# Performance work log

Measured on AMD Instinct MI355X. Metric: run time of the kernel, lower is better.

The kernel has to match this reference:

```python
import jax, jax.numpy as jnp
import numpy as np

N_EMBD = 1024
N_HEAD = 16
BASE_SCALE = 0.03125  # config.base_scale
ATTN_ALPHA_INIT = 0.05
MLP_ALPHA_INIT = 0.05
SQK_INIT = 1.0
SUV_INIT = 1.0


def justnorm(x):
    return x / jnp.linalg.norm(x, axis=-1, keepdims=True)


def normalized_linear(x, W):
    # F.normalize(weight, p=2, dim=0): unit-norm columns of W [out, in] across the out dim
    Wn = W / jnp.linalg.norm(W, axis=0, keepdims=True)
    return x @ Wn.T


def setup_inputs() -> dict:
    key = jax.random.key(0)
    ks = jax.random.split(key, 8)
    C = N_EMBD
    s = 1.0 / np.sqrt(C)
    inp = {
        "h": jax.random.normal(ks[0], (8, 1024, C), dtype=jnp.float32),
        "Wq": jax.random.normal(ks[1], (C, C), dtype=jnp.float32) * s,
        "Wk": jax.random.normal(ks[2], (C, C), dtype=jnp.float32) * s,
        "Wv": jax.random.normal(ks[3], (C, C), dtype=jnp.float32) * s,
        "Wo": jax.random.normal(ks[4], (C, C), dtype=jnp.float32) * s,
        "Wfc": jax.random.normal(ks[5], (8 * C, C), dtype=jnp.float32) * s,
        "Wproj": jax.random.normal(ks[6], (C, 4 * C), dtype=jnp.float32) * (1.0 / np.sqrt(4 * C)),
        "sqk": jnp.full((C,), SQK_INIT * BASE_SCALE, dtype=jnp.float32),
        "suv": jnp.full((8 * C,), SUV_INIT * 1.0, dtype=jnp.float32),
        "attn_alpha": jnp.full((C,), BASE_SCALE, dtype=jnp.float32),
        "mlp_alpha": jnp.full((C,), BASE_SCALE, dtype=jnp.float32),
    }
    return inp


def reference(h, Wq, Wk, Wv, Wo, Wfc, Wproj, sqk, suv, attn_alpha, mlp_alpha):
    B, T, C = h.shape
    H, D = N_HEAD, C // N_HEAD

    # ---- attention ----
    q = normalized_linear(h, Wq).reshape(B, T, H, D).transpose(0, 2, 1, 3)  # bhtd
    k = normalized_linear(h, Wk).reshape(B, T, H, D).transpose(0, 2, 1, 3)
    v = normalized_linear(h, Wv).reshape(B, T, H, D).transpose(0, 2, 1, 3)

    sqk_s = (sqk * (SQK_INIT / BASE_SCALE)).reshape(1, H, 1, D)  # per-(head, head_dim) scale
    q = sqk_s * justnorm(q)
    k = sqk_s * justnorm(k)

    softmax_scale = float(D) ** 0.5  # nGPT uses sqrt(head_dim)
    att = jax.nn.softmax(jnp.einsum("bhqd,bhkd->bhqk", q, k) * softmax_scale, axis=-1)
    y = jnp.einsum("bhqk,bhkd->bhqd", att, v)
    y = y.transpose(0, 2, 1, 3).reshape(B, T, C)
    h_att = normalized_linear(y, Wo)

    lr = jnp.abs(attn_alpha * (ATTN_ALPHA_INIT / BASE_SCALE))
    A = justnorm(h)
    Bn = justnorm(h_att)
    h = justnorm(A + lr * (Bn - A))

    # ---- SwiGLU MLP ----
    uv = h @ Wfc.T  # [B,T,8C]
    suv_s = suv * (SUV_INIT / 1.0 * (C ** 0.5))
    uv = suv_s * uv
    u, vg = jnp.split(uv, 2, axis=-1)
    x_mlp = u * jax.nn.silu(vg)
    h_mlp = x_mlp @ Wproj.T

    lr = jnp.abs(mlp_alpha * (MLP_ALPHA_INIT / BASE_SCALE))
    A = justnorm(h)
    Bn = justnorm(h_mlp)
    h = justnorm(A + lr * (Bn - A))
    return h
```

## Files before the change

### kernel.cpp

```cpp
#include <hip/hip_runtime.h>

typedef __attribute__((ext_vector_type(8))) short s8v;
typedef __attribute__((ext_vector_type(4))) short s4v;
typedef __attribute__((ext_vector_type(4))) float f4v;

__device__ __forceinline__ float b2f(unsigned short b) {
  union { unsigned u; float f; } x; x.u = ((unsigned)b) << 16; return x.f;
}
__device__ __forceinline__ unsigned short f2b(float f) {
  union { float f; unsigned u; } x; x.f = f;
  unsigned r = x.u + 0x7fffu + ((x.u >> 16) & 1u);
  return (unsigned short)(r >> 16);
}
__device__ __forceinline__ void gl_lds16(const void* g, void* l) {
  __builtin_amdgcn_global_load_lds(
      (const __attribute__((address_space(1))) unsigned int*)g,
      (__attribute__((address_space(3))) unsigned int*)l, 16, 0, 0);
}

__global__ void colsq(const float* __restrict__ W, float* __restrict__ out, int K) {
  int j = blockIdx.x * 256 + threadIdx.x;
  const float* p = W + (long)(blockIdx.y * 64) * K + j;
  float s = 0.f;
#pragma unroll 4
  for (int n = 0; n < 64; ++n) { float v = p[(long)n * K]; s += v * v; }
  atomicAdd(&out[j], s);
}

__global__ void convw(const float* __restrict__ src, const float* __restrict__ cs,
                      unsigned short* __restrict__ dst, int Kmask) {
  long idx = ((long)blockIdx.x * 256 + threadIdx.x) << 2;
  float4 v = *(const float4*)(src + idx);
  int j = (int)(idx & (long)Kmask);
  s4v o;
  o[0] = (short)f2b(v.x * rsqrtf(cs[j]));
  o[1] = (short)f2b(v.y * rsqrtf(cs[j + 1]));
  o[2] = (short)f2b(v.z * rsqrtf(cs[j + 2]));
  o[3] = (short)f2b(v.w * rsqrtf(cs[j + 3]));
  *(s4v*)(dst + idx) = o;
}

__global__ void castf2b(const float* __restrict__ src, unsigned short* __restrict__ dst) {
  long idx = ((long)blockIdx.x * 256 + threadIdx.x) << 2;
  float4 v = *(const float4*)(src + idx);
  s4v o;
  o[0] = (short)f2b(v.x); o[1] = (short)f2b(v.y);
  o[2] = (short)f2b(v.z); o[3] = (short)f2b(v.w);
  *(s4v*)(dst + idx) = o;
}

__global__ __launch_bounds__(256) void gemm_bt(
    const unsigned short* __restrict__ A, const unsigned short* __restrict__ B,
    unsigned short* __restrict__ Cout, int K, int ldc) {
  __shared__ unsigned short smem[32768];
  const int tid = threadIdx.x, lane = tid & 63, w = tid >> 6;
  const int quad = lane >> 4, lq = lane & 15;
  const int wy = w >> 1, wx = w & 1;
  const int m0 = blockIdx.y << 7, n0 = blockIdx.x << 7;

  const int trow = tid >> 2;
  const int cb = ((tid & 3) ^ ((tid >> 3) & 3)) << 3;
  const unsigned short* Ag0 = A + (long)(m0 + trow) * K + cb;
  const unsigned short* Ag1 = A + (long)(m0 + 64 + trow) * K + cb;
  const unsigned short* Bg0 = B + (long)(n0 + trow) * K + cb;
  const unsigned short* Bg1 = B + (long)(n0 + 64 + trow) * K + cb;
  unsigned short* l0 = smem + (tid << 3);

  const int swz = ((lq >> 1) & 3) << 4;
  const int aoff = (wy * 64 + lq) * 64 + ((quad << 4) ^ swz);
  const int boff = 8192 + (wx * 64 + lq) * 64 + ((quad << 4) ^ swz);

  f4v acc[4][4];
  f4v zero = {0.f, 0.f, 0.f, 0.f};
#pragma unroll
  for (int i = 0; i < 4; ++i)
#pragma unroll
    for (int j = 0; j < 4; ++j) acc[i][j] = zero;

  auto stage = [&](int T) {
    const int bo = (T & 3) << 13;
    const int col = T << 5;
    gl_lds16(Ag0 + col, l0 + bo);
    gl_lds16(Ag1 + col, l0 + bo + 2048);
    gl_lds16(Bg0 + col, l0 + bo + 4096);
    gl_lds16(Bg1 + col, l0 + bo + 6144);
  };
  const char* sb = (const char*)smem;
  auto compute = [&](int kt) {
    const int bo = (kt & 3) << 14;
    s8v a[4], b[4];
#pragma unroll
    for (int i = 0; i < 4; ++i) a[i] = *(const s8v*)(sb + bo + aoff + i * 1024);
#pragma unroll
    for (int j = 0; j < 4; ++j) b[j] = *(const s8v*)(sb + bo + boff + j * 1024);
    __builtin_amdgcn_s_setprio(1);
#pragma unroll
    for (int i = 0; i < 4; ++i)
#pragma unroll
      for (int j = 0; j < 4; ++j)
        acc[i][j] = __builtin_amdgcn_mfma_f32_16x16x32_bf16(a[i], b[j], acc[i][j], 0, 0, 0);
    __builtin_amdgcn_s_setprio(0);
  };

  const int nt = K >> 5;
  stage(0); stage(1); stage(2);
  for (int kt = 0; kt < nt - 2; ++kt) {
    asm volatile("s_waitcnt vmcnt(8)" ::: "memory");
    __builtin_amdgcn_s_barrier();
    asm volatile("" ::: "memory");
    if (kt < nt - 3) stage(kt + 3);
    compute(kt);
  }
  asm volatile("s_waitcnt vmcnt(4)" ::: "memory");
  __builtin_amdgcn_s_barrier();
  asm volatile("" ::: "memory");
  compute(nt - 2);
  asm volatile("s_waitcnt vmcnt(0)" ::: "memory");
  __builtin_amdgcn_s_barrier();
  asm volatile("" ::: "memory");
  compute(nt - 1);

  __syncthreads();
#pragma unroll
  for (int i = 0; i < 4; ++i)
#pragma unroll
    for (int j = 0; j < 4; ++j)
#pragma unroll
      for (int r = 0; r < 4; ++r) {
        int row = wy * 64 + i * 16 + quad * 4 + r;
        int col = wx * 64 + j * 16 + lq;
        smem[row * 136 + col] = f2b(acc[i][j][r]);
      }
  __syncthreads();
#pragma unroll
  for (int it = 0; it < 8; ++it) {
    int row = it * 16 + (tid >> 4);
    int col = (tid & 15) << 3;
    s8v v = *(const s8v*)(smem + row * 136 + col);
    *(s8v*)(Cout + (long)(m0 + row) * ldc + n0 + col) = v;
  }
}

__global__ __launch_bounds__(512, 2) void gemm_fc(
    const unsigned short* __restrict__ A, const unsigned short* __restrict__ B,
    unsigned short* __restrict__ X, const float* __restrict__ suv) {
  __shared__ unsigned short smem[65536];
  const int tid = threadIdx.x, lane = tid & 63, w = tid >> 6;
  const int quad = lane >> 4, lq = lane & 15;
  const int wy = w >> 2, wx = w & 3;
  const int bid = blockIdx.x;
  const int xr = bid & 7, xq = bid >> 3;
  const int m0 = ((xr << 2) | (xq & 3)) << 8;
  const int n0 = (xq >> 2) << 7;

  const int swz = ((lq >> 1) & 3) << 4;
  const int aoff = wy * 8192 + lq * 64 + ((quad * 16) ^ swz);
  const int boff = 16384 + wx * 2048 + lq * 64 + ((quad * 16) ^ swz);

  const int trow = tid >> 2;
  const int cb = ((tid & 3) ^ ((tid >> 3) & 3)) << 3;
  const unsigned short* Ag0 = A + (long)(m0 + trow) * 1024 + cb;
  const unsigned short* Ag1 = A + (long)(m0 + 128 + trow) * 1024 + cb;
  const unsigned short* Bg0 = B + (long)(n0 + trow) * 1024 + cb;
  const unsigned short* Bg1 = B + (long)(4096 + n0 + trow) * 1024 + cb;
  unsigned short* l0 = smem + (tid << 3);

  float su[2], sv[2];
#pragma unroll
  for (int j = 0; j < 2; ++j) {
    su[j] = suv[n0 + wx * 32 + j * 16 + lq] * 32.f;
    sv[j] = suv[4096 + n0 + wx * 32 + j * 16 + lq] * 32.f;
  }

  f4v aU[8][2], aV[8][2];
  f4v zero = {0.f, 0.f, 0.f, 0.f};
#pragma unroll
  for (int m = 0; m < 8; ++m)
#pragma unroll
    for (int j = 0; j < 2; ++j) { aU[m][j] = zero; aV[m][j] = zero; }

  auto stage = [&](int T) {
    const int bo = (T & 3) << 14;
    const int col = T << 5;
    gl_lds16(Ag0 + col, l0 + bo);
    gl_lds16(Ag1 + col, l0 + bo + 4096);
    gl_lds16(Bg0 + col, l0 + bo + 8192);
    gl_lds16(Bg1 + col, l0 + bo + 12288);
  };

  const char* sb = (const char*)smem;
  auto compute = [&](int kt) {
    const int bo = (kt & 3) << 15;
    s8v bu0 = *(const s8v*)(sb + bo + boff);
    s8v bu1 = *(const s8v*)(sb + bo + boff + 1024);
    s8v bv0 = *(const s8v*)(sb + bo + boff + 8192);
    s8v bv1 = *(const s8v*)(sb + bo + boff + 9216);
    s8v av[8];
#pragma unroll
    for (int m = 0; m < 8; ++m) av[m] = *(const s8v*)(sb + bo + aoff + m * 1024);
    __builtin_amdgcn_s_setprio(1);
#pragma unroll
    for (int m = 0; m < 8; ++m) {
      aU[m][0] = __builtin_amdgcn_mfma_f32_16x16x32_bf16(av[m], bu0, aU[m][0], 0, 0, 0);
      aV[m][0] = __builtin_amdgcn_mfma_f32_16x16x32_bf16(av[m], bv0, aV[m][0], 0, 0, 0);
      aU[m][1] = __builtin_amdgcn_mfma_f32_16x16x32_bf16(av[m], bu1, aU[m][1], 0, 0, 0);
      aV[m][1] = __builtin_amdgcn_mfma_f32_16x16x32_bf16(av[m], bv1, aV[m][1], 0, 0, 0);
    }
    __builtin_amdgcn_s_setprio(0);
  };

  stage(0); stage(1); stage(2);
  for (int kt = 0; kt < 30; ++kt) {
    asm volatile("s_waitcnt vmcnt(8)" ::: "memory");
    __builtin_amdgcn_s_barrier();
    asm volatile("" ::: "memory");
    if (kt < 29) stage(kt + 3);
    compute(kt);
  }
  asm volatile("s_waitcnt vmcnt(4)" ::: "memory");
  __builtin_amdgcn_s_barrier();
  asm volatile("" ::: "memory");
  compute(30);
  asm volatile("s_waitcnt vmcnt(0)" ::: "memory");
  __builtin_amdgcn_s_barrier();
  asm volatile("" ::: "memory");
  compute(31);

  __syncthreads();
#pragma unroll
  for (int m = 0; m < 8; ++m)
#pragma unroll
    for (int j = 0; j < 2; ++j)
#pragma unroll
      for (int r = 0; r < 4; ++r) {
        int row = wy * 128 + m * 16 + quad * 4 + r;
        int col = wx * 32 + j * 16 + lq;
        float uu = aU[m][j][r] * su[j];
        float vg = aV[m][j][r] * sv[j];
        float sig = 1.f / (1.f + __builtin_amdgcn_exp2f(vg * -1.44269504f));
        smem[row * 132 + col] = f2b(uu * vg * sig);
      }
  __syncthreads();
  {
    const int row = tid >> 1, half = tid & 1;
    unsigned short* dst = X + (long)(m0 + row) * 4096 + n0 + half * 64;
    const unsigned short* srcr = smem + row * 132 + half * 64;
#pragma unroll
    for (int s = 0; s < 8; ++s)
      *(s8v*)(dst + s * 8) = *(const s8v*)(srcr + s * 8);
  }
}

__global__ __launch_bounds__(256) void qkv_norm(unsigned short* __restrict__ qkv,
                                                unsigned short* __restrict__ Vt,
                                                const float* __restrict__ sqk) {
  __shared__ unsigned short tl[64][72];
  const int tid = threadIdx.x;
  const int blk = blockIdx.x;
  const int tt = blk & 15, bh = blk >> 4, b = bh >> 4, h = bh & 15;
  const int t0 = tt << 6;
  const int r = tid >> 2, seg = tid & 3;
  float sc[16];
#pragma unroll
  for (int c = 0; c < 16; ++c) sc[c] = sqk[h * 64 + seg * 16 + c] * 32.f;
  for (int which = 0; which < 2; ++which) {
    unsigned short* p = qkv + (long)(b * 1024 + t0 + r) * 3072 + which * 1024 + h * 64 + seg * 16;
    s8v x0 = *(const s8v*)p, x1 = *(const s8v*)(p + 8);
    float ss = 0.f;
#pragma unroll
    for (int c = 0; c < 8; ++c) {
      float a = b2f((unsigned short)x0[c]), bb = b2f((unsigned short)x1[c]);
      ss += a * a + bb * bb;
    }
    ss += __shfl_xor(ss, 1, 64);
    ss += __shfl_xor(ss, 2, 64);
    float rn = rsqrtf(ss);
#pragma unroll
    for (int c = 0; c < 8; ++c) {
      x0[c] = (short)f2b(b2f((unsigned short)x0[c]) * rn * sc[c]);
      x1[c] = (short)f2b(b2f((unsigned short)x1[c]) * rn * sc[c + 8]);
    }
    *(s8v*)p = x0; *(s8v*)(p + 8) = x1;
  }
  {
    const unsigned short* p = qkv + (long)(b * 1024 + t0 + r) * 3072 + 2048 + h * 64 + seg * 16;
    s8v v0 = *(const s8v*)p, v1 = *(const s8v*)(p + 8);
#pragma unroll
    for (int c = 0; c < 8; ++c) {
      tl[seg * 16 + c][r] = (unsigned short)v0[c];
      tl[seg * 16 + 8 + c][r] = (unsigned short)v1[c];
    }
  }
  __syncthreads();
  {
    const int d = tid >> 2, part = tid & 3;
    s8v o0 = *(const s8v*)(&tl[d][part * 16]);
    s8v o1 = *(const s8v*)(&tl[d][part * 16 + 8]);
    unsigned short* q = Vt + (long)(bh * 64 + d) * 1024 + t0 + part * 16;
    *(s8v*)q = o0; *(s8v*)(q + 8) = o1;
  }
}

__global__ __launch_bounds__(256) void attn(const unsigned short* __restrict__ qkv,
                                            const unsigned short* __restrict__ Vt,
                                            unsigned short* __restrict__ Y) {
  __shared__ unsigned short smem[33792];
  unsigned short* Klds = smem;
  unsigned short* Vlds = smem + 8192;
  unsigned short* Plds = smem + 16384;
  const int tid = threadIdx.x, lane = tid & 63, w = tid >> 6;
  const int quad = lane >> 4, lq = lane & 15;
  const int bh = blockIdx.x, b = bh >> 4, h = bh & 15;
  const int qt = blockIdx.y;
  const int e0 = tid << 3;
  const int c_lo = e0 >> 10, row_s = (e0 & 1023) >> 3;
  const int vc_lo = e0 >> 9, vd = (e0 & 511) >> 3;

  s8v qf[2][2];
#pragma unroll
  for (int i = 0; i < 2; ++i)
#pragma unroll
    for (int ks = 0; ks < 2; ++ks) {
      int row = qt * 128 + w * 32 + i * 16 + lq;
      qf[i][ks] = *(const s8v*)(qkv + (long)(b * 1024 + row) * 3072 + h * 64 + ks * 32 + quad * 8);
    }

  f4v o[2][4];
  float lp[2][4];
  f4v zero = {0.f, 0.f, 0.f, 0.f};
#pragma unroll
  for (int i = 0; i < 2; ++i) {
#pragma unroll
    for (int nf = 0; nf < 4; ++nf) o[i][nf] = zero;
#pragma unroll
    for (int r = 0; r < 4; ++r) lp[i][r] = 0.f;
  }

  const unsigned short* Kg = qkv + (long)(b * 1024 + row_s) * 3072 + 1024 + h * 64 + (c_lo << 3);
  const unsigned short* Vg = Vt + (long)(bh * 64 + vd) * 1024 + (vc_lo << 3);
  unsigned short* Pw = Plds + w * 4352;

  for (int kt0 = 0; kt0 < 1024; kt0 += 128) {
    __syncthreads();
#pragma unroll
    for (int it = 0; it < 4; ++it) {
      gl_lds16(Kg + (long)kt0 * 3072 + it * 16, Klds + it * 2048 + e0);
      gl_lds16(Vg + kt0 + it * 32, Vlds + it * 2048 + e0);
    }
    __syncthreads();
    f4v s[2][8];
#pragma unroll
    for (int i = 0; i < 2; ++i)
#pragma unroll
      for (int j = 0; j < 8; ++j) s[i][j] = zero;
#pragma unroll
    for (int ks = 0; ks < 2; ++ks)
#pragma unroll
      for (int j = 0; j < 8; ++j) {
        s8v kf = *(const s8v*)(Klds + (ks * 4 + quad) * 1024 + (j * 16 + lq) * 8);
        s[0][j] = __builtin_amdgcn_mfma_f32_16x16x32_bf16(qf[0][ks], kf, s[0][j], 0, 0, 0);
        s[1][j] = __builtin_amdgcn_mfma_f32_16x16x32_bf16(qf[1][ks], kf, s[1][j], 0, 0, 0);
      }
#pragma unroll
    for (int i = 0; i < 2; ++i)
#pragma unroll
      for (int j = 0; j < 8; ++j)
#pragma unroll
        for (int r = 0; r < 4; ++r) {
          float p = __builtin_amdgcn_exp2f(s[i][j][r] * 11.5415603f - 11.5415603f);
          lp[i][r] += p;
          Pw[(i * 16 + quad * 4 + r) * 136 + j * 16 + lq] = f2b(p);
        }
    s8v pf[2][4];
#pragma unroll
    for (int i = 0; i < 2; ++i)
#pragma unroll
      for (int ks = 0; ks < 4; ++ks)
        pf[i][ks] = *(const s8v*)(Pw + (i * 16 + lq) * 136 + ks * 32 + quad * 8);
#pragma unroll
    for (int nf = 0; nf < 4; ++nf)
#pragma unroll
      for (int ks = 0; ks < 4; ++ks) {
        s8v vf = *(const s8v*)(Vlds + (ks * 4 + quad) * 512 + (nf * 16 + lq) * 8);
        o[0][nf] = __builtin_amdgcn_mfma_f32_16x16x32_bf16(pf[0][ks], vf, o[0][nf], 0, 0, 0);
        o[1][nf] = __builtin_amdgcn_mfma_f32_16x16x32_bf16(pf[1][ks], vf, o[1][nf], 0, 0, 0);
      }
  }
#pragma unroll
  for (int i = 0; i < 2; ++i)
#pragma unroll
    for (int r = 0; r < 4; ++r) {
      float v = lp[i][r];
      v += __shfl_xor(v, 1, 64); v += __shfl_xor(v, 2, 64);
      v += __shfl_xor(v, 4, 64); v += __shfl_xor(v, 8, 64);
      lp[i][r] = 1.f / v;
    }
#pragma unroll
  for (int i = 0; i < 2; ++i)
#pragma unroll
    for (int nf = 0; nf < 4; ++nf)
#pragma unroll
      for (int r = 0; r < 4; ++r) {
        int row = qt * 128 + w * 32 + i * 16 + quad * 4 + r;
        Y[(long)(b * 1024 + row) * 1024 + h * 64 + nf * 16 + lq] = f2b(o[i][nf][r] * lp[i][r]);
      }
}

__global__ __launch_bounds__(256) void residual(
    const float* __restrict__ hin, const unsigned short* __restrict__ hbr,
    const float* __restrict__ alpha, float* __restrict__ outf,
    unsigned short* __restrict__ outb) {
  __shared__ float red[8];
  const int tid = threadIdx.x, lane = tid & 63, w = tid >> 6;
  const long base = (long)blockIdx.x * 1024;
  float hv[4], bvv[4];
  float s1 = 0.f, s2 = 0.f;
#pragma unroll
  for (int k = 0; k < 4; ++k) {
    int c = k * 256 + tid;
    hv[k] = hin[base + c];
    bvv[k] = b2f(hbr[base + c]);
    s1 += hv[k] * hv[k]; s2 += bvv[k] * bvv[k];
  }
#pragma unroll
  for (int m = 1; m < 64; m <<= 1) { s1 += __shfl_xor(s1, m, 64); s2 += __shfl_xor(s2, m, 64); }
  if (lane == 0) { red[w] = s1; red[4 + w] = s2; }
  __syncthreads();
  s1 = red[0] + red[1] + red[2] + red[3];
  s2 = red[4] + red[5] + red[6] + red[7];
  float rn1 = rsqrtf(s1), rn2 = rsqrtf(s2);
  float z[4], s3 = 0.f;
#pragma unroll
  for (int k = 0; k < 4; ++k) {
    int c = k * 256 + tid;
    float a = hv[k] * rn1;
    float lr = fabsf(alpha[c]) * 1.6f;
    float zz = a + lr * (bvv[k] * rn2 - a);
    z[k] = zz; s3 += zz * zz;
  }
#pragma unroll
  for (int m = 1; m < 64; m <<= 1) s3 += __shfl_xor(s3, m, 64);
  __syncthreads();
  if (lane == 0) red[w] = s3;
  __syncthreads();
  s3 = red[0] + red[1] + red[2] + red[3];
  float rn3 = rsqrtf(s3);
#pragma unroll
  for (int k = 0; k < 4; ++k) {
    int c = k * 256 + tid;
    float ov = z[k] * rn3;
    if (outf) outf[base + c] = ov;
    if (outb) outb[base + c] = f2b(ov);
  }
}

extern "C" void kernel_launch(void* const* d_in, const int* in_sizes, int n_in,
                              void* d_out, int out_size, void* d_ws, size_t ws_size,
                              hipStream_t stream) {
  const float* h   = (const float*)d_in[0];
  const float* Wq  = (const float*)d_in[1];
  const float* Wk  = (const float*)d_in[2];
  const float* Wv  = (const float*)d_in[3];
  const float* Wo  = (const float*)d_in[4];
  const float* Wfc = (const float*)d_in[5];
  const float* Wpj = (const float*)d_in[6];
  const float* sqk = (const float*)d_in[7];
  const float* suv = (const float*)d_in[8];
  const float* aat = (const float*)d_in[9];
  const float* aml = (const float*)d_in[10];
  float* out = (float*)d_out;

  char* ws = (char*)d_ws;
  size_t off = 0;
  auto alloc = [&](size_t n) { char* p = ws + off; off += (n + 255) & ~(size_t)255; return p; };
  float* cs_q  = (float*)alloc(4096);
  float* cs_k  = (float*)alloc(4096);
  float* cs_v  = (float*)alloc(4096);
  float* cs_o  = (float*)alloc(4096);
  unsigned short* Wqkv_b = (unsigned short*)alloc(3ull * 1024 * 1024 * 2);
  unsigned short* Wo_b   = (unsigned short*)alloc(1024ull * 1024 * 2);
  unsigned short* Wfc_b  = (unsigned short*)alloc(8192ull * 1024 * 2);
  unsigned short* Wpj_b  = (unsigned short*)alloc(1024ull * 4096 * 2);
  unsigned short* slotC  = (unsigned short*)alloc(8192ull * 1024 * 2);
  unsigned short* slotD  = (unsigned short*)alloc(8192ull * 4096 * 2);
  unsigned short* slotE  = (unsigned short*)alloc(8192ull * 1024 * 2);
  unsigned short* y_b    = (unsigned short*)alloc(8192ull * 1024 * 2);
  float*          h2_f   = (float*)alloc(8192ull * 1024 * 4);

  unsigned short* h_b    = slotC;
  unsigned short* hmlp_b = slotC;
  unsigned short* qkv_r  = slotD;
  unsigned short* xmlp   = slotD;
  unsigned short* hatt_b = slotD + 25165824;
  unsigned short* Vt     = slotE;
  unsigned short* h2_b   = slotE;

  hipMemsetAsync(ws, 0, 16384, stream);
  colsq<<<dim3(4, 16), 256, 0, stream>>>(Wq, cs_q, 1024);
  colsq<<<dim3(4, 16), 256, 0, stream>>>(Wk, cs_k, 1024);
  colsq<<<dim3(4, 16), 256, 0, stream>>>(Wv, cs_v, 1024);
  colsq<<<dim3(4, 16), 256, 0, stream>>>(Wo, cs_o, 1024);
  convw<<<1024, 256, 0, stream>>>(Wq, cs_q, Wqkv_b, 1023);
  convw<<<1024, 256, 0, stream>>>(Wk, cs_k, Wqkv_b + 1048576, 1023);
  convw<<<1024, 256, 0, stream>>>(Wv, cs_v, Wqkv_b + 2097152, 1023);
  convw<<<1024, 256, 0, stream>>>(Wo, cs_o, Wo_b, 1023);
  castf2b<<<8192, 256, 0, stream>>>(Wfc, Wfc_b);
  castf2b<<<4096, 256, 0, stream>>>(Wpj, Wpj_b);
  castf2b<<<8192, 256, 0, stream>>>(h, h_b);
  gemm_bt<<<dim3(24, 64), 256, 0, stream>>>(h_b, Wqkv_b, qkv_r, 1024, 3072);
  qkv_norm<<<2048, 256, 0, stream>>>(qkv_r, Vt, sqk);
  attn<<<dim3(128, 8), 256, 0, stream>>>(qkv_r, Vt, y_b);
  gemm_bt<<<dim3(8, 64), 256, 0, stream>>>(y_b, Wo_b, hatt_b, 1024, 1024);
  residual<<<8192, 256, 0, stream>>>(h, hatt_b, aat, h2_f, h2_b);
  gemm_fc<<<1024, 512, 0, stream>>>(h2_b, Wfc_b, xmlp, suv);
  gemm_bt<<<dim3(8, 64), 256, 0, stream>>>(xmlp, Wpj_b, hmlp_b, 4096, 1024);
  residual<<<8192, 256, 0, stream>>>(h2_f, hmlp_b, aml, out, nullptr);
}
```

Measured before the change: 649.6 us.

## Restructure gemm_fc into 64-wide K tiles with four-phase ping-pong LDS pipeline

The fc GEMM mainloop goes from a 4-stage ring of 32-wide K tiles to two 64-wide K-tile buffers. Each tile is processed in four phases (U/V times two M halves), and global-to-LDS loads for later tiles are interleaved between the MFMA phases, separated by barriers. It also changes the LDS swizzle to an 8-way XOR over 128-byte rows to reduce bank conflicts. The aim is to overlap loads with compute at a finer grain and halve the loop iterations, at the cost of many more barriers and a tighter vmcnt accounting that could stall or be fragile.

```diff
diff --git a/kernel.cpp b/kernel.cpp
--- a/kernel.cpp
+++ b/kernel.cpp
@@ -3,6 +3,8 @@
 typedef __attribute__((ext_vector_type(8))) short s8v;
 typedef __attribute__((ext_vector_type(4))) short s4v;
 typedef __attribute__((ext_vector_type(4))) float f4v;
+
+#define MFMA __builtin_amdgcn_mfma_f32_16x16x32_bf16
 
 __device__ __forceinline__ float b2f(unsigned short b) {
   union { unsigned u; float f; } x; x.u = ((unsigned)b) << 16; return x.f;
@@ -98,7 +100,7 @@
     for (int i = 0; i < 4; ++i)
 #pragma unroll
       for (int j = 0; j < 4; ++j)
-        acc[i][j] = __builtin_amdgcn_mfma_f32_16x16x32_bf16(a[i], b[j], acc[i][j], 0, 0, 0);
+        acc[i][j] = MFMA(a[i], b[j], acc[i][j], 0, 0, 0);
     __builtin_amdgcn_s_setprio(0);
   };
 
@@ -153,17 +155,137 @@
   const int m0 = ((xr << 2) | (xq & 3)) << 8;
   const int n0 = (xq >> 2) << 7;
 
-  const int swz = ((lq >> 1) & 3) << 4;
-  const int aoff = wy * 8192 + lq * 64 + ((quad * 16) ^ swz);
-  const int boff = 16384 + wx * 2048 + lq * 64 + ((quad * 16) ^ swz);
-
-  const int trow = tid >> 2;
-  const int cb = ((tid & 3) ^ ((tid >> 3) & 3)) << 3;
-  const unsigned short* Ag0 = A + (long)(m0 + trow) * 1024 + cb;
-  const unsigned short* Ag1 = A + (long)(m0 + 128 + trow) * 1024 + cb;
-  const unsigned short* Bg0 = B + (long)(n0 + trow) * 1024 + cb;
-  const unsigned short* Bg1 = B + (long)(4096 + n0 + trow) * 1024 + cb;
-  unsigned short* l0 = smem + (tid << 3);
+  const int trow = tid >> 3;
+  const int scol = ((tid & 7) ^ (trow & 7)) << 3;
+  const unsigned short* pA = A + (long)(m0 + trow) * 1024 + scol;
+  const unsigned short* pB = B + (long)(n0 + trow) * 1024 + scol;
+  unsigned short* ldst = smem + tid * 8;
+
+  auto stA = [&](int tile, int half) {
+    const int base = (tile & 1) * 32768 + half * 8192;
+    const unsigned short* src = pA + (long)half * 131072 + (tile << 6);
+    gl_lds16(src, ldst + base);
+    gl_lds16(src + 65536, ldst + base + 4096);
+  };
+  auto stB = [&](int tile, int vh) {
+    const int base = (tile & 1) * 32768 + 16384 + vh * 8192;
+    const unsigned short* src = pB + (long)vh * 4194304 + (tile << 6);
+    gl_lds16(src, ldst + base);
+    gl_lds16(src + 65536, ldst + base + 4096);
+  };
+
+  const int rsw = (lq & 7) << 4;
+  const int c0 = (quad * 16) ^ rsw;
+  const int c1 = (64 + quad * 16) ^ rsw;
+  const int aro = wy * 16384 + lq * 128;
+  const int uro = 32768 + (wx * 32 + lq) * 128;
+  const int vro = 49152 + (wx * 32 + lq) * 128;
+  const char* sb = (const char*)smem;
+
+  f4v aU[8][2], aV[8][2];
+  f4v zero = {0.f, 0.f, 0.f, 0.f};
+#pragma unroll
+  for (int m = 0; m < 8; ++m)
+#pragma unroll
+    for (int j = 0; j < 2; ++j) { aU[m][j] = zero; aV[m][j] = zero; }
+
+  s8v av[4][2], uf[2][2], vg[2][2];
+
+  auto tile_phases = [&](int t, int bufB) {
+#pragma unroll
+    for (int m = 0; m < 4; ++m) {
+      av[m][0] = *(const s8v*)(sb + bufB + aro + m * 2048 + c0);
+      av[m][1] = *(const s8v*)(sb + bufB + aro + m * 2048 + c1);
+    }
+#pragma unroll
+    for (int j = 0; j < 2; ++j) {
+      uf[j][0] = *(const s8v*)(sb + bufB + uro + j * 2048 + c0);
+      uf[j][1] = *(const s8v*)(sb + bufB + uro + j * 2048 + c1);
+    }
+    if (t < 15) stA(t + 1, 1);
+    __builtin_amdgcn_s_barrier();
+    asm volatile("" ::: "memory");
+    __builtin_amdgcn_s_setprio(1);
+#pragma unroll
+    for (int m = 0; m < 4; ++m)
+#pragma unroll
+      for (int j = 0; j < 2; ++j) {
+        aU[m][j] = MFMA(av[m][0], uf[j][0], aU[m][j], 0, 0, 0);
+        aU[m][j] = MFMA(av[m][1], uf[j][1], aU[m][j], 0, 0, 0);
+      }
+    __builtin_amdgcn_s_setprio(0);
+    asm volatile("" ::: "memory");
+    __builtin_amdgcn_s_barrier();
+    asm volatile("" ::: "memory");
+#pragma unroll
+    for (int j = 0; j < 2; ++j) {
+      vg[j][0] = *(const s8v*)(sb + bufB + vro + j * 2048 + c0);
+      vg[j][1] = *(const s8v*)(sb + bufB + vro + j * 2048 + c1);
+    }
+    if (t < 14) stB(t + 2, 0);
+    __builtin_amdgcn_s_barrier();
+    asm volatile("" ::: "memory");
+    __builtin_amdgcn_s_setprio(1);
+#pragma unroll
+    for (int m = 0; m < 4; ++m)
+#pragma unroll
+      for (int j = 0; j < 2; ++j) {
+        aV[m][j] = MFMA(av[m][0], vg[j][0], aV[m][j], 0, 0, 0);
+        aV[m][j] = MFMA(av[m][1], vg[j][1], aV[m][j], 0, 0, 0);
+      }
+    __builtin_amdgcn_s_setprio(0);
+    asm volatile("" ::: "memory");
+    __builtin_amdgcn_s_barrier();
+    asm volatile("" ::: "memory");
+#pragma unroll
+    for (int m = 0; m < 4; ++m) {
+      av[m][0] = *(const s8v*)(sb + bufB + aro + (m + 4) * 2048 + c0);
+      av[m][1] = *(const s8v*)(sb + bufB + aro + (m + 4) * 2048 + c1);
+    }
+    if (t < 14) stB(t + 2, 1);
+    __builtin_amdgcn_s_barrier();
+    asm volatile("" ::: "memory");
+    __builtin_amdgcn_s_setprio(1);
+#pragma unroll
+    for (int m = 0; m < 4; ++m)
+#pragma unroll
+      for (int j = 0; j < 2; ++j) {
+        aU[m + 4][j] = MFMA(av[m][0], uf[j][0], aU[m + 4][j], 0, 0, 0);
+        aU[m + 4][j] = MFMA(av[m][1], uf[j][1], aU[m + 4][j], 0, 0, 0);
+      }
+    __builtin_amdgcn_s_setprio(0);
+    asm volatile("" ::: "memory");
+    __builtin_amdgcn_s_barrier();
+    asm volatile("" ::: "memory");
+    if (t < 14) stA(t + 2, 0);
+    __builtin_amdgcn_s_barrier();
+    asm volatile("" ::: "memory");
+    __builtin_amdgcn_s_setprio(1);
+#pragma unroll
+    for (int m = 0; m < 4; ++m)
+#pragma unroll
+      for (int j = 0; j < 2; ++j) {
+        aV[m + 4][j] = MFMA(av[m][0], vg[j][0], aV[m + 4][j], 0, 0, 0);
+        aV[m + 4][j] = MFMA(av[m][1], vg[j][1], aV[m + 4][j], 0, 0, 0);
+      }
+    __builtin_amdgcn_s_setprio(0);
+    if (t < 14) { asm volatile("s_waitcnt vmcnt(6)" ::: "memory"); }
+    else if (t == 14) { asm volatile("s_waitcnt vmcnt(0)" ::: "memory"); }
+    asm volatile("" ::: "memory");
+    __builtin_amdgcn_s_barrier();
+    asm volatile("" ::: "memory");
+  };
+
+  stB(0, 0); stB(0, 1); stA(0, 0); stA(0, 1);
+  stB(1, 0); stB(1, 1); stA(1, 0);
+  asm volatile("s_waitcnt vmcnt(6)" ::: "memory");
+  __builtin_amdgcn_s_barrier();
+  asm volatile("" ::: "memory");
+
+  for (int tt = 0; tt < 8; ++tt) {
+    tile_phases(tt * 2, 0);
+    tile_phases(tt * 2 + 1, 65536);
+  }
 
   float su[2], sv[2];
 #pragma unroll
@@ -171,61 +293,6 @@
     su[j] = suv[n0 + wx * 32 + j * 16 + lq] * 32.f;
     sv[j] = suv[4096 + n0 + wx * 32 + j * 16 + lq] * 32.f;
   }
-
-  f4v aU[8][2], aV[8][2];
-  f4v zero = {0.f, 0.f, 0.f, 0.f};
-#pragma unroll
-  for (int m = 0; m < 8; ++m)
-#pragma unroll
-    for (int j = 0; j < 2; ++j) { aU[m][j] = zero; aV[m][j] = zero; }
-
-  auto stage = [&](int T) {
-    const int bo = (T & 3) << 14;
-    const int col = T << 5;
-    gl_lds16(Ag0 + col, l0 + bo);
-    gl_lds16(Ag1 + col, l0 + bo + 4096);
-    gl_lds16(Bg0 + col, l0 + bo + 8192);
-    gl_lds16(Bg1 + col, l0 + bo + 12288);
-  };
-
-  const char* sb = (const char*)smem;
-  auto compute = [&](int kt) {
-    const int bo = (kt & 3) << 15;
-    s8v bu0 = *(const s8v*)(sb + bo + boff);
-    s8v bu1 = *(const s8v*)(sb + bo + boff + 1024);
-    s8v bv0 = *(const s8v*)(sb + bo + boff + 8192);
-    s8v bv1 = *(const s8v*)(sb + bo + boff + 9216);
-    s8v av[8];
-#pragma unroll
-    for (int m = 0; m < 8; ++m) av[m] = *(const s8v*)(sb + bo + aoff + m * 1024);
-    __builtin_amdgcn_s_setprio(1);
-#pragma unroll
-    for (int m = 0; m < 8; ++m) {
-      aU[m][0] = __builtin_amdgcn_mfma_f32_16x16x32_bf16(av[m], bu0, aU[m][0], 0, 0, 0);
-      aV[m][0] = __builtin_amdgcn_mfma_f32_16x16x32_bf16(av[m], bv0, aV[m][0], 0, 0, 0);
-      aU[m][1] = __builtin_amdgcn_mfma_f32_16x16x32_bf16(av[m], bu1, aU[m][1], 0, 0, 0);
-      aV[m][1] = __builtin_amdgcn_mfma_f32_16x16x32_bf16(av[m], bv1, aV[m][1], 0, 0, 0);
-    }
-    __builtin_amdgcn_s_setprio(0);
-  };
-
-  stage(0); stage(1); stage(2);
-  for (int kt = 0; kt < 30; ++kt) {
-    asm volatile("s_waitcnt vmcnt(8)" ::: "memory");
-    __builtin_amdgcn_s_barrier();
-    asm volatile("" ::: "memory");
-    if (kt < 29) stage(kt + 3);
-    compute(kt);
-  }
-  asm volatile("s_waitcnt vmcnt(4)" ::: "memory");
-  __builtin_amdgcn_s_barrier();
-  asm volatile("" ::: "memory");
-  compute(30);
-  asm volatile("s_waitcnt vmcnt(0)" ::: "memory");
-  __builtin_amdgcn_s_barrier();
-  asm volatile("" ::: "memory");
-  compute(31);
-
   __syncthreads();
 #pragma unroll
   for (int m = 0; m < 8; ++m)
@@ -236,9 +303,9 @@
         int row = wy * 128 + m * 16 + quad * 4 + r;
         int col = wx * 32 + j * 16 + lq;
         float uu = aU[m][j][r] * su[j];
-        float vg = aV[m][j][r] * sv[j];
-        float sig = 1.f / (1.f + __builtin_amdgcn_exp2f(vg * -1.44269504f));
-        smem[row * 132 + col] = f2b(uu * vg * sig);
+        float vv = aV[m][j][r] * sv[j];
+        float sig = 1.f / (1.f + __builtin_amdgcn_exp2f(vv * -1.44269504f));
+        smem[row * 132 + col] = f2b(uu * vv * sig);
       }
   __syncthreads();
   {
@@ -358,8 +425,8 @@
 #pragma unroll
       for (int j = 0; j < 8; ++j) {
         s8v kf = *(const s8v*)(Klds + (ks * 4 + quad) * 1024 + (j * 16 + lq) * 8);
-        s[0][j] = __builtin_amdgcn_mfma_f32_16x16x32_bf16(qf[0][ks], kf, s[0][j], 0, 0, 0);
-        s[1][j] = __builtin_amdgcn_mfma_f32_16x16x32_bf16(qf[1][ks], kf, s[1][j], 0, 0, 0);
+        s[0][j] = MFMA(qf[0][ks], kf, s[0][j], 0, 0, 0);
+        s[1][j] = MFMA(qf[1][ks], kf, s[1][j], 0, 0, 0);
       }
 #pragma unroll
     for (int i = 0; i < 2; ++i)
@@ -382,8 +449,8 @@
 #pragma unroll
       for (int ks = 0; ks < 4; ++ks) {
         s8v vf = *(const s8v*)(Vlds + (ks * 4 + quad) * 512 + (nf * 16 + lq) * 8);
-        o[0][nf] = __builtin_amdgcn_mfma_f32_16x16x32_bf16(pf[0][ks], vf, o[0][nf], 0, 0, 0);
-        o[1][nf] = __builtin_amdgcn_mfma_f32_16x16x32_bf16(pf[1][ks], vf, o[1][nf], 0, 0, 0);
+        o[0][nf] = MFMA(pf[0][ks], vf, o[0][nf], 0, 0, 0);
+        o[1][nf] = MFMA(pf[1][ks], vf, o[1][nf], 0, 0, 0);
       }
   }
 #pragma unroll
```

Result: no change. 642.1 us (-1.2%).
